# Kernel optimization log

Hardware: AMD Instinct MI355X
Metric: run time of the kernel (lower is better)

Reference implementation:

```python
import jax, jax.numpy as jnp
import numpy as np

B, C = 1, 1
D = H = W = 128          # volume depth/height/width (z, y, x)
V = U = 128              # detector rows (v) / cols (u)
A = 96                   # projection angles
N_STEPS = 128            # Joseph ray-marching steps
SX = SY = SD = 1.0       # voxel size (sd, sy, sx)
SU = SV = 1.0            # detector spacing (sv, su)


def setup_inputs() -> dict:
    key = jax.random.key(0)
    # model-facing volume [B, C, X, Y, Z]
    vol = jax.random.normal(key, (B, C, W, H, D), dtype=jnp.float32)
    angles = jnp.linspace(0.0, np.pi, A, endpoint=False).astype(jnp.float32)
    return {"vol": vol, "angles": angles}


def _corner(idx, size):
    """Floor/ceil corner indices + zero-padded linear weights (align_corners=True,
    padding_mode='zeros' semantics of F.grid_sample)."""
    i0f = jnp.floor(idx)
    frac = idx - i0f
    i0 = i0f.astype(jnp.int32)
    i1 = i0 + 1
    w0 = jnp.where((i0 >= 0) & (i0 < size), 1.0 - frac, 0.0)
    w1 = jnp.where((i1 >= 0) & (i1 < size), frac, 0.0)
    return jnp.clip(i0, 0, size - 1), jnp.clip(i1, 0, size - 1), w0, w1


def reference(vol, angles):
    # [B,C,X,Y,Z] -> [B,C,D,H,W] (z,y,x ordering used internally)
    v_zyx = jnp.transpose(vol, (0, 1, 4, 3, 2))
    cos_t = jnp.cos(angles)[:, None]   # [A,1]
    sin_t = jnp.sin(angles)[:, None]   # [A,1]
    u = (jnp.arange(U, dtype=jnp.float32) - (U - 1) / 2.0) * SU   # [U]
    v = (jnp.arange(V, dtype=jnp.float32) - (V - 1) / 2.0) * SV   # [V]
    # half ray length = half in-plane diagonal
    T = 0.5 * float(np.sqrt(((W - 1) * SX) ** 2 + ((H - 1) * SY) ** 2))
    delta_t = 2.0 * T / float(N_STEPS)

    x_base = -u[None, :] * sin_t   # [A,U] ray point at t=0
    y_base = u[None, :] * cos_t    # [A,U]
    # z depends only on detector row v; constant along the ray
    z_idx = v / SD + (D - 1) / 2.0                     # [V]
    z0, z1, wz0, wz1 = _corner(z_idx, D)
    z0, z1 = z0[:, None], z1[:, None]                  # [V,1]
    wz0, wz1 = wz0[:, None], wz1[:, None]

    t_vals = -T + (jnp.arange(N_STEPS, dtype=jnp.float32) + 0.5) * delta_t

    def step(acc, t):
        x_idx = (x_base + t * cos_t) / SX + (W - 1) / 2.0   # [A,U]
        y_idx = (y_base + t * sin_t) / SY + (H - 1) / 2.0   # [A,U]
        x0, x1, wx0, wx1 = [a[:, None, :] for a in _corner(x_idx, W)]  # [A,1,U]
        y0, y1, wy0, wy1 = [a[:, None, :] for a in _corner(y_idx, H)]  # [A,1,U]
        g = lambda zi, yi, xi: v_zyx[:, :, zi, yi, xi]      # -> [B,C,A,V,U]
        s = (wz0 * (wy0 * (wx0 * g(z0, y0, x0) + wx1 * g(z0, y0, x1))
                    + wy1 * (wx0 * g(z0, y1, x0) + wx1 * g(z0, y1, x1)))
             + wz1 * (wy0 * (wx0 * g(z1, y0, x0) + wx1 * g(z1, y0, x1))
                      + wy1 * (wx0 * g(z1, y1, x0) + wx1 * g(z1, y1, x1))))
        return acc + s, None

    acc0 = jnp.zeros((B, C, A, V, U), dtype=vol.dtype)
    acc, _ = jax.lax.scan(jax.checkpoint(step), acc0, t_vals)
    sino = acc * jnp.float32(delta_t)            # [B,C,A,V,U]
    # model-facing sinogram [B,C,X=U,A,Z=V]
    return jnp.transpose(sino, (0, 1, 4, 2, 3))
```

## Files before the change

kernel.cpp:

```cpp
#include <hip/hip_runtime.h>
#include <hip/hip_fp16.h>

namespace {
constexpr int A_N = 96;
constexpr int U_N = 128;
constexpr int V_N = 128;
constexpr int W_N = 128;
constexpr int H_N = 128;
constexpr int NSTEPS = 128;
constexpr float T_HALF = 89.80256121069154f;
constexpr float DT = 1.4031650189170554f;
constexpr float INV_DT = 1.0f / DT;
constexpr int PAD = 6;
constexpr int WP = W_N + 2 * PAD;
constexpr int ROW_BYTES = WP * 256;
constexpr int ZT = 8;
constexpr int RAYS_PER_BLOCK = 16;
constexpr int BLOCK_THREADS = RAYS_PER_BLOCK * ZT;
constexpr size_t VOLP_COLS = (size_t)WP * WP;
constexpr size_t VOLP_BYTES = VOLP_COLS * 256;
constexpr size_t SINO = (size_t)U_N * A_N * V_N;
}

__device__ __forceinline__ unsigned int packh2(float a, float b) {
    return (unsigned int)__half_as_ushort(__float2half_rn(a)) |
           ((unsigned int)__half_as_ushort(__float2half_rn(b)) << 16);
}

__global__ __launch_bounds__(256) void vol_pad_f16(
    const float* __restrict__ vol, unsigned int* __restrict__ volp)
{
    const int idx = blockIdx.x * 256 + threadIdx.x;
    if (idx >= (int)(VOLP_COLS * 16)) return;
    const int zo  = idx & 15;
    const int col = idx >> 4;
    const int yp = col % WP;
    const int xp = col / WP;
    const int x = xp - PAD;
    const int y = yp - PAD;
    uint4 o = make_uint4(0u, 0u, 0u, 0u);
    if ((unsigned)x < 128u && (unsigned)y < 128u) {
        const float* src = vol + (((size_t)x * 128 + y) << 7) + zo * 8;
        const float4 f0 = *(const float4*)(src);
        const float4 f1 = *(const float4*)(src + 4);
        o.x = packh2(f0.x, f0.y);
        o.y = packh2(f0.z, f0.w);
        o.z = packh2(f1.x, f1.y);
        o.w = packh2(f1.z, f1.w);
    }
    *(uint4*)((char*)volp + (size_t)col * 256 + zo * 16) = o;
}

__device__ __forceinline__ const char* step_base(
    const char* volc, int laneb, float i_f, float cv, float sv, float xb, float yb,
    float& fx, float& fy)
{
    const float tf = fmaf(i_f + 0.5f, DT, -T_HALF);
    const float xi = fmaf(tf, cv, xb);
    const float yi = fmaf(tf, sv, yb);
    const float fx0 = floorf(xi);
    const float fy0 = floorf(yi);
    fx = xi - fx0;
    fy = yi - fy0;
    const int x0 = (int)fx0;
    const int y0 = (int)fy0;
    const int base = (((x0 + PAD) * WP + (y0 + PAD)) << 8) + laneb;
    return volc + base;
}

__device__ __forceinline__ void consume16(
    const uint4* q, float fx, float fy, __half2* hacc)
{
    const float wx0 = 1.f - fx;
    const float wy0 = 1.f - fy;
    const __half2 w00 = __float2half2_rn(wx0 * wy0);
    const __half2 w01 = __float2half2_rn(wx0 * fy);
    const __half2 w10 = __float2half2_rn(fx  * wy0);
    const __half2 w11 = __float2half2_rn(fx  * fy);
    const __half2* h00 = (const __half2*)&q[0];
    const __half2* h01 = (const __half2*)&q[2];
    const __half2* h10 = (const __half2*)&q[4];
    const __half2* h11 = (const __half2*)&q[6];
#pragma unroll
    for (int j = 0; j < 8; ++j) {
        hacc[j] = __hfma2(w00, h00[j], hacc[j]);
        hacc[j] = __hfma2(w01, h01[j], hacc[j]);
        hacc[j] = __hfma2(w10, h10[j], hacc[j]);
        hacc[j] = __hfma2(w11, h11[j], hacc[j]);
    }
}

__global__ __launch_bounds__(BLOCK_THREADS, 4) void joseph_fwd_inc(
    const unsigned short* __restrict__ volp,
    const float* __restrict__ angles,
    float* __restrict__ dst, float scale)
{
    const int zo = threadIdx.x & (ZT - 1);
    const int r  = threadIdx.x >> 3;
    const int bx = (int)blockIdx.x;
    const int xt = (bx & 1) ? (4 + (bx >> 1)) : (3 - (bx >> 1));
    const int u_i = xt * RAYS_PER_BLOCK + r;
    const int a   = blockIdx.y;

    const int spseg = NSTEPS / gridDim.z;
    const int i0 = blockIdx.z * spseg;
    const int i1 = i0 + spseg;

    const float ang = angles[a];
    const float cv = cosf(ang);
    const float sv = sinf(ang);
    const float up = (float)u_i - 63.5f;
    const float xb = fmaf(-up, sv, 63.5f);
    const float yb = fmaf( up, cv, 63.5f);

    float tlo = -2.f * T_HALF, thi = 2.f * T_HALF;
    if (fabsf(cv) > 1e-6f) {
        const float ta = (-1.f - xb) / cv, tb = (128.f - xb) / cv;
        tlo = fmaxf(tlo, fminf(ta, tb));
        thi = fminf(thi, fmaxf(ta, tb));
    } else if (xb <= -1.f || xb >= 128.f) { thi = tlo - 1.f; }
    if (fabsf(sv) > 1e-6f) {
        const float ta = (-1.f - yb) / sv, tb = (128.f - yb) / sv;
        tlo = fmaxf(tlo, fminf(ta, tb));
        thi = fminf(thi, fmaxf(ta, tb));
    } else if (yb <= -1.f || yb >= 128.f) { thi = tlo - 1.f; }
    const int ilo = (int)floorf(fmaf(tlo + T_HALF, INV_DT, -0.5f)) - 1;
    const int ihi = (int)ceilf (fmaf(thi + T_HALF, INV_DT, -0.5f)) + 1;
    int lo = min(max(ilo, i0), i1);
    int hi = min(max(ihi + 1, i0), i1);
    lo &= ~1;
    hi = (hi + 1) & ~1;

    const char* __restrict__ volc = (const char*)volp;
    const int laneb = zo << 5;

    __half2 hacc[8];
    float accf[16];
#pragma unroll
    for (int j = 0; j < 8; ++j) hacc[j] = __float2half2_rn(0.f);
#pragma unroll
    for (int k = 0; k < 16; ++k) accf[k] = 0.f;

    int kc = 0;
    for (int i = lo; i < hi; i += 2) {
        float fxA, fyA, fxB, fyB;
        const char* pA = step_base(volc, laneb, (float)i,       cv, sv, xb, yb, fxA, fyA);
        const char* pB = step_base(volc, laneb, (float)(i + 1), cv, sv, xb, yb, fxB, fyB);

        uint4 qA[8], qB[8];
        qA[0] = *(const uint4*)(pA);
        qA[1] = *(const uint4*)(pA + 16);
        qA[2] = *(const uint4*)(pA + 256);
        qA[3] = *(const uint4*)(pA + 272);
        qA[4] = *(const uint4*)(pA + ROW_BYTES);
        qA[5] = *(const uint4*)(pA + ROW_BYTES + 16);
        qA[6] = *(const uint4*)(pA + ROW_BYTES + 256);
        qA[7] = *(const uint4*)(pA + ROW_BYTES + 272);
        qB[0] = *(const uint4*)(pB);
        qB[1] = *(const uint4*)(pB + 16);
        qB[2] = *(const uint4*)(pB + 256);
        qB[3] = *(const uint4*)(pB + 272);
        qB[4] = *(const uint4*)(pB + ROW_BYTES);
        qB[5] = *(const uint4*)(pB + ROW_BYTES + 16);
        qB[6] = *(const uint4*)(pB + ROW_BYTES + 256);
        qB[7] = *(const uint4*)(pB + ROW_BYTES + 272);

        consume16(qA, fxA, fyA, hacc);
        consume16(qB, fxB, fyB, hacc);

        if (((++kc) & 1) == 0) {
#pragma unroll
            for (int j = 0; j < 8; ++j) {
                const float2 f = __half22float2(hacc[j]);
                accf[2 * j]     += f.x;
                accf[2 * j + 1] += f.y;
                hacc[j] = __float2half2_rn(0.f);
            }
        }
    }
#pragma unroll
    for (int j = 0; j < 8; ++j) {
        const float2 f = __half22float2(hacc[j]);
        accf[2 * j]     += f.x;
        accf[2 * j + 1] += f.y;
    }

    float* op = dst + (size_t)blockIdx.z * SINO + ((size_t)u_i * A_N + a) * V_N + 16 * zo;
    *(float4*)(op)      = make_float4(accf[0]  * scale, accf[1]  * scale, accf[2]  * scale, accf[3]  * scale);
    *(float4*)(op + 4)  = make_float4(accf[4]  * scale, accf[5]  * scale, accf[6]  * scale, accf[7]  * scale);
    *(float4*)(op + 8)  = make_float4(accf[8]  * scale, accf[9]  * scale, accf[10] * scale, accf[11] * scale);
    *(float4*)(op + 12) = make_float4(accf[12] * scale, accf[13] * scale, accf[14] * scale, accf[15] * scale);
}

__global__ __launch_bounds__(256) void reduce_segs(
    const float4* __restrict__ p, float4* __restrict__ out, int nseg)
{
    const size_t i = (size_t)blockIdx.x * 256 + threadIdx.x;
    const size_t q = SINO / 4;
    float4 s = p[i];
    for (int k = 1; k < nseg; ++k) {
        const float4 b = p[i + (size_t)k * q];
        s.x += b.x; s.y += b.y; s.z += b.z; s.w += b.w;
    }
    out[i] = make_float4(s.x * DT, s.y * DT, s.z * DT, s.w * DT);
}

__global__ __launch_bounds__(256) void joseph_fwd_f32(
    const float* __restrict__ vol,
    const float* __restrict__ angles,
    float* __restrict__ out)
{
    const int zo  = threadIdx.x & 15;
    const int r   = threadIdx.x >> 4;
    const int u_i = blockIdx.x * 16 + r;
    const int a   = blockIdx.y;

    const float ang = angles[a];
    const float c = cosf(ang);
    const float s = sinf(ang);
    const float u = (float)u_i - 63.5f;
    const float xb = fmaf(-u, s, 63.5f);
    const float yb = fmaf( u, c, 63.5f);

    const float* volz = vol + 8 * zo;
    float4 accA = make_float4(0.f, 0.f, 0.f, 0.f);
    float4 accB = make_float4(0.f, 0.f, 0.f, 0.f);

    for (int i = 0; i < NSTEPS; ++i) {
        const float t  = fmaf((float)i + 0.5f, DT, -T_HALF);
        const float xi = fmaf(t, c, xb);
        const float yi = fmaf(t, s, yb);
        const float fx0f = floorf(xi);
        const float fy0f = floorf(yi);
        const int x0 = (int)fx0f;
        const int y0 = (int)fy0f;
        const float fx = xi - fx0f;
        const float fy = yi - fy0f;
        const int x1 = x0 + 1;
        const int y1 = y0 + 1;
        const float wx0 = (x0 >= 0 && x0 < W_N) ? (1.f - fx) : 0.f;
        const float wx1 = (x1 >= 0 && x1 < W_N) ? fx : 0.f;
        const float wy0 = (y0 >= 0 && y0 < H_N) ? (1.f - fy) : 0.f;
        const float wy1 = (y1 >= 0 && y1 < H_N) ? fy : 0.f;
        if ((wx0 + wx1) == 0.f || (wy0 + wy1) == 0.f) continue;
        const int cx0 = min(max(x0, 0), W_N - 1);
        const int cx1 = min(max(x1, 0), W_N - 1);
        const int cy0 = min(max(y0, 0), H_N - 1);
        const int cy1 = min(max(y1, 0), H_N - 1);
        const float* p00 = volz + ((cx0 * H_N + cy0) << 7);
        const float* p01 = volz + ((cx1 * H_N + cy0) << 7);
        const float* p10 = volz + ((cx0 * H_N + cy1) << 7);
        const float* p11 = volz + ((cx1 * H_N + cy1) << 7);
        const float4 v00a = *(const float4*)(p00);
        const float4 v00b = *(const float4*)(p00 + 4);
        const float4 v01a = *(const float4*)(p01);
        const float4 v01b = *(const float4*)(p01 + 4);
        const float4 v10a = *(const float4*)(p10);
        const float4 v10b = *(const float4*)(p10 + 4);
        const float4 v11a = *(const float4*)(p11);
        const float4 v11b = *(const float4*)(p11 + 4);
        const float w00 = wx0 * wy0, w01 = wx1 * wy0, w10 = wx0 * wy1, w11 = wx1 * wy1;
        accA.x = fmaf(w00, v00a.x, fmaf(w01, v01a.x, fmaf(w10, v10a.x, fmaf(w11, v11a.x, accA.x))));
        accA.y = fmaf(w00, v00a.y, fmaf(w01, v01a.y, fmaf(w10, v10a.y, fmaf(w11, v11a.y, accA.y))));
        accA.z = fmaf(w00, v00a.z, fmaf(w01, v01a.z, fmaf(w10, v10a.z, fmaf(w11, v11a.z, accA.z))));
        accA.w = fmaf(w00, v00a.w, fmaf(w01, v01a.w, fmaf(w10, v10a.w, fmaf(w11, v11a.w, accA.w))));
        accB.x = fmaf(w00, v00b.x, fmaf(w01, v01b.x, fmaf(w10, v10b.x, fmaf(w11, v11b.x, accB.x))));
        accB.y = fmaf(w00, v00b.y, fmaf(w01, v01b.y, fmaf(w10, v10b.y, fmaf(w11, v11b.y, accB.y))));
        accB.z = fmaf(w00, v00b.z, fmaf(w01, v01b.z, fmaf(w10, v10b.z, fmaf(w11, v11b.z, accB.z))));
        accB.w = fmaf(w00, v00b.w, fmaf(w01, v01b.w, fmaf(w10, v10b.w, fmaf(w11, v11b.w, accB.w))));
    }

    float* op = out + ((size_t)u_i * A_N + a) * V_N + 8 * zo;
    *(float4*)(op)     = make_float4(accA.x * DT, accA.y * DT, accA.z * DT, accA.w * DT);
    *(float4*)(op + 4) = make_float4(accB.x * DT, accB.y * DT, accB.z * DT, accB.w * DT);
}

extern "C" void kernel_launch(void* const* d_in, const int* in_sizes, int n_in,
                              void* d_out, int out_size, void* d_ws, size_t ws_size,
                              hipStream_t stream) {
    const float* vol    = (const float*)d_in[0];
    const float* angles = (const float*)d_in[1];
    float* out          = (float*)d_out;

    const int pad_blocks = (int)((VOLP_COLS * 16 + 255) / 256);

    if (ws_size >= VOLP_BYTES) {
        unsigned int* volp = (unsigned int*)d_ws;
        hipLaunchKernelGGL(vol_pad_f16, dim3(pad_blocks), dim3(256), 0, stream, vol, volp);

        int nseg = 0;
        if (ws_size >= VOLP_BYTES + 4 * SINO * sizeof(float))      nseg = 4;
        else if (ws_size >= VOLP_BYTES + 2 * SINO * sizeof(float)) nseg = 2;

        if (nseg) {
            float* partial = (float*)((char*)d_ws + VOLP_BYTES);
            dim3 grid(U_N / RAYS_PER_BLOCK, A_N, nseg);
            hipLaunchKernelGGL(joseph_fwd_inc, grid, dim3(BLOCK_THREADS), 0, stream,
                               (const unsigned short*)volp, angles, partial, 1.0f);
            hipLaunchKernelGGL(reduce_segs, dim3(SINO / 4 / 256), dim3(256), 0, stream,
                               (const float4*)partial, (float4*)out, nseg);
        } else {
            dim3 grid(U_N / RAYS_PER_BLOCK, A_N, 1);
            hipLaunchKernelGGL(joseph_fwd_inc, grid, dim3(BLOCK_THREADS), 0, stream,
                               (const unsigned short*)volp, angles, out, DT);
        }
    } else {
        dim3 grid(U_N / 16, A_N);
        hipLaunchKernelGGL(joseph_fwd_f32, grid, dim3(256), 0, stream, vol, angles, out);
    }
}
```

Baseline: 121.7 us.

## Software-pipeline Joseph step loads and interleave z lanes for coalesced access

Restructures the ray-march loop into a two-stage software pipeline: loads for the next step are issued before the current step's half-precision FMAs run, so load latency is hidden behind compute. The per-thread z slice changes from 16 contiguous halves to two 8-half chunks at 64-half stride (lane offset zo*16 bytes). Adjacent lanes now read contiguous 16-byte pieces, and the output stores are remapped to match. This adds register pressure from holding two steps' worth of loads in flight.

```diff
diff --git a/kernel.cpp b/kernel.cpp
--- a/kernel.cpp
+++ b/kernel.cpp
@@ -51,45 +51,6 @@
     *(uint4*)((char*)volp + (size_t)col * 256 + zo * 16) = o;
 }
 
-__device__ __forceinline__ const char* step_base(
-    const char* volc, int laneb, float i_f, float cv, float sv, float xb, float yb,
-    float& fx, float& fy)
-{
-    const float tf = fmaf(i_f + 0.5f, DT, -T_HALF);
-    const float xi = fmaf(tf, cv, xb);
-    const float yi = fmaf(tf, sv, yb);
-    const float fx0 = floorf(xi);
-    const float fy0 = floorf(yi);
-    fx = xi - fx0;
-    fy = yi - fy0;
-    const int x0 = (int)fx0;
-    const int y0 = (int)fy0;
-    const int base = (((x0 + PAD) * WP + (y0 + PAD)) << 8) + laneb;
-    return volc + base;
-}
-
-__device__ __forceinline__ void consume16(
-    const uint4* q, float fx, float fy, __half2* hacc)
-{
-    const float wx0 = 1.f - fx;
-    const float wy0 = 1.f - fy;
-    const __half2 w00 = __float2half2_rn(wx0 * wy0);
-    const __half2 w01 = __float2half2_rn(wx0 * fy);
-    const __half2 w10 = __float2half2_rn(fx  * wy0);
-    const __half2 w11 = __float2half2_rn(fx  * fy);
-    const __half2* h00 = (const __half2*)&q[0];
-    const __half2* h01 = (const __half2*)&q[2];
-    const __half2* h10 = (const __half2*)&q[4];
-    const __half2* h11 = (const __half2*)&q[6];
-#pragma unroll
-    for (int j = 0; j < 8; ++j) {
-        hacc[j] = __hfma2(w00, h00[j], hacc[j]);
-        hacc[j] = __hfma2(w01, h01[j], hacc[j]);
-        hacc[j] = __hfma2(w10, h10[j], hacc[j]);
-        hacc[j] = __hfma2(w11, h11[j], hacc[j]);
-    }
-}
-
 __global__ __launch_bounds__(BLOCK_THREADS, 4) void joseph_fwd_inc(
     const unsigned short* __restrict__ volp,
     const float* __restrict__ angles,
@@ -132,7 +93,7 @@
     hi = (hi + 1) & ~1;
 
     const char* __restrict__ volc = (const char*)volp;
-    const int laneb = zo << 5;
+    const int laneb = zo << 4;
 
     __half2 hacc[8];
     float accf[16];
@@ -141,55 +102,114 @@
 #pragma unroll
     for (int k = 0; k < 16; ++k) accf[k] = 0.f;
 
-    int kc = 0;
-    for (int i = lo; i < hi; i += 2) {
-        float fxA, fyA, fxB, fyB;
-        const char* pA = step_base(volc, laneb, (float)i,       cv, sv, xb, yb, fxA, fyA);
-        const char* pB = step_base(volc, laneb, (float)(i + 1), cv, sv, xb, yb, fxB, fyB);
-
-        uint4 qA[8], qB[8];
-        qA[0] = *(const uint4*)(pA);
-        qA[1] = *(const uint4*)(pA + 16);
-        qA[2] = *(const uint4*)(pA + 256);
-        qA[3] = *(const uint4*)(pA + 272);
-        qA[4] = *(const uint4*)(pA + ROW_BYTES);
-        qA[5] = *(const uint4*)(pA + ROW_BYTES + 16);
-        qA[6] = *(const uint4*)(pA + ROW_BYTES + 256);
-        qA[7] = *(const uint4*)(pA + ROW_BYTES + 272);
-        qB[0] = *(const uint4*)(pB);
-        qB[1] = *(const uint4*)(pB + 16);
-        qB[2] = *(const uint4*)(pB + 256);
-        qB[3] = *(const uint4*)(pB + 272);
-        qB[4] = *(const uint4*)(pB + ROW_BYTES);
-        qB[5] = *(const uint4*)(pB + ROW_BYTES + 16);
-        qB[6] = *(const uint4*)(pB + ROW_BYTES + 256);
-        qB[7] = *(const uint4*)(pB + ROW_BYTES + 272);
-
-        consume16(qA, fxA, fyA, hacc);
-        consume16(qB, fxB, fyB, hacc);
-
-        if (((++kc) & 1) == 0) {
+    uint4 A0, A1, A2, A3, A4, A5, A6, A7;
+    uint4 B0, B1, B2, B3, B4, B5, B6, B7;
+    float fxA, fyA, fxB, fyB;
+
+    auto base_of = [&](float i_f, float& fx, float& fy) -> const char* {
+        const float tf = fmaf(i_f + 0.5f, DT, -T_HALF);
+        const float xi = fmaf(tf, cv, xb);
+        const float yi = fmaf(tf, sv, yb);
+        const float fx0 = floorf(xi);
+        const float fy0 = floorf(yi);
+        fx = xi - fx0;
+        fy = yi - fy0;
+        const int x0 = (int)fx0;
+        const int y0 = (int)fy0;
+        return volc + ((((x0 + PAD) * WP + (y0 + PAD)) << 8) + laneb);
+    };
+
+    auto issueA = [&](int i) {
+        const char* p = base_of((float)i, fxA, fyA);
+        const char* p2 = p + ROW_BYTES;
+        A0 = *(const uint4*)(p);
+        A1 = *(const uint4*)(p + 128);
+        A2 = *(const uint4*)(p + 256);
+        A3 = *(const uint4*)(p + 384);
+        A4 = *(const uint4*)(p2);
+        A5 = *(const uint4*)(p2 + 128);
+        A6 = *(const uint4*)(p2 + 256);
+        A7 = *(const uint4*)(p2 + 384);
+    };
+    auto issueB = [&](int i) {
+        const char* p = base_of((float)i, fxB, fyB);
+        const char* p2 = p + ROW_BYTES;
+        B0 = *(const uint4*)(p);
+        B1 = *(const uint4*)(p + 128);
+        B2 = *(const uint4*)(p + 256);
+        B3 = *(const uint4*)(p + 384);
+        B4 = *(const uint4*)(p2);
+        B5 = *(const uint4*)(p2 + 128);
+        B6 = *(const uint4*)(p2 + 256);
+        B7 = *(const uint4*)(p2 + 384);
+    };
+
+    auto consume = [&](const uint4& q00l, const uint4& q00h, const uint4& q01l, const uint4& q01h,
+                       const uint4& q10l, const uint4& q10h, const uint4& q11l, const uint4& q11h,
+                       float fx, float fy) {
+        const float wx0 = 1.f - fx;
+        const float wy0 = 1.f - fy;
+        const __half2 w00 = __float2half2_rn(wx0 * wy0);
+        const __half2 w01 = __float2half2_rn(wx0 * fy);
+        const __half2 w10 = __float2half2_rn(fx  * wy0);
+        const __half2 w11 = __float2half2_rn(fx  * fy);
+        const __half2* h00l = (const __half2*)&q00l;
+        const __half2* h01l = (const __half2*)&q01l;
+        const __half2* h10l = (const __half2*)&q10l;
+        const __half2* h11l = (const __half2*)&q11l;
+        const __half2* h00h = (const __half2*)&q00h;
+        const __half2* h01h = (const __half2*)&q01h;
+        const __half2* h10h = (const __half2*)&q10h;
+        const __half2* h11h = (const __half2*)&q11h;
 #pragma unroll
-            for (int j = 0; j < 8; ++j) {
-                const float2 f = __half22float2(hacc[j]);
-                accf[2 * j]     += f.x;
-                accf[2 * j + 1] += f.y;
-                hacc[j] = __float2half2_rn(0.f);
+        for (int j = 0; j < 4; ++j) {
+            hacc[j] = __hfma2(w00, h00l[j], hacc[j]);
+            hacc[j] = __hfma2(w01, h01l[j], hacc[j]);
+            hacc[j] = __hfma2(w10, h10l[j], hacc[j]);
+            hacc[j] = __hfma2(w11, h11l[j], hacc[j]);
+            hacc[4 + j] = __hfma2(w00, h00h[j], hacc[4 + j]);
+            hacc[4 + j] = __hfma2(w01, h01h[j], hacc[4 + j]);
+            hacc[4 + j] = __hfma2(w10, h10h[j], hacc[4 + j]);
+            hacc[4 + j] = __hfma2(w11, h11h[j], hacc[4 + j]);
+        }
+    };
+
+    auto flush = [&]() {
+#pragma unroll
+        for (int j = 0; j < 8; ++j) {
+            const float2 f = __half22float2(hacc[j]);
+            accf[2 * j]     += f.x;
+            accf[2 * j + 1] += f.y;
+            hacc[j] = __float2half2_rn(0.f);
+        }
+    };
+
+    if (lo < hi) {
+        int kc = 0;
+        int i = lo;
+        issueA(i);
+        for (;;) {
+            issueB(i + 1);
+            consume(A0, A1, A2, A3, A4, A5, A6, A7, fxA, fyA);
+            i += 2;
+            if (i >= hi) {
+                consume(B0, B1, B2, B3, B4, B5, B6, B7, fxB, fyB);
+                break;
             }
+            issueA(i);
+            consume(B0, B1, B2, B3, B4, B5, B6, B7, fxB, fyB);
+            if (((++kc) & 1) == 0) flush();
         }
     }
-#pragma unroll
-    for (int j = 0; j < 8; ++j) {
-        const float2 f = __half22float2(hacc[j]);
-        accf[2 * j]     += f.x;
-        accf[2 * j + 1] += f.y;
-    }
-
-    float* op = dst + (size_t)blockIdx.z * SINO + ((size_t)u_i * A_N + a) * V_N + 16 * zo;
-    *(float4*)(op)      = make_float4(accf[0]  * scale, accf[1]  * scale, accf[2]  * scale, accf[3]  * scale);
-    *(float4*)(op + 4)  = make_float4(accf[4]  * scale, accf[5]  * scale, accf[6]  * scale, accf[7]  * scale);
-    *(float4*)(op + 8)  = make_float4(accf[8]  * scale, accf[9]  * scale, accf[10] * scale, accf[11] * scale);
-    *(float4*)(op + 12) = make_float4(accf[12] * scale, accf[13] * scale, accf[14] * scale, accf[15] * scale);
+    flush();
+
+    float* op = dst + (size_t)blockIdx.z * SINO + ((size_t)u_i * A_N + a) * V_N;
+    float* opl = op + 8 * zo;
+    float* oph = op + 64 + 8 * zo;
+    *(float4*)(opl)     = make_float4(accf[0]  * scale, accf[1]  * scale, accf[2]  * scale, accf[3]  * scale);
+    *(float4*)(opl + 4) = make_float4(accf[4]  * scale, accf[5]  * scale, accf[6]  * scale, accf[7]  * scale);
+    *(float4*)(oph)     = make_float4(accf[8]  * scale, accf[9]  * scale, accf[10] * scale, accf[11] * scale);
+    *(float4*)(oph + 4) = make_float4(accf[12] * scale, accf[13] * scale, accf[14] * scale, accf[15] * scale);
 }
 
 __global__ __launch_bounds__(256) void reduce_segs(
```

After: 117.8 us. -3.2%, faster.
